# Kernel tuning notes

Measured on AMD Instinct MI355X. Metric: run time of the kernel, lower is better.

## Reference

```python
import jax, jax.numpy as jnp
import numpy as np

NEG_SLOPE = 0.2  # PyG GATConv default


def _gat_conv(x, src, dst, W, a_src, a_dst, bias, concat):
    # x: [N, F_in]; W: [H*C, F_in]; a_src/a_dst: [H, C]; src/dst: [E]
    n = x.shape[0]
    H, C = a_src.shape
    h = (x @ W.T).reshape(n, H, C)                       # [N, H, C]
    al_src = (h * a_src[None]).sum(-1)                   # [N, H]
    al_dst = (h * a_dst[None]).sum(-1)                   # [N, H]
    e = jax.nn.leaky_relu(al_src[src] + al_dst[dst], NEG_SLOPE)  # [E, H]
    # scatter-softmax over incoming edges of each dst node
    m = jax.ops.segment_max(e, dst, num_segments=n)      # [N, H]
    e = jnp.exp(e - m[dst])
    denom = jax.ops.segment_sum(e, dst, num_segments=n)  # [N, H]
    alpha = e / denom[dst]                               # [E, H]
    out = jax.ops.segment_sum(alpha[:, :, None] * h[src], dst, num_segments=n)  # [N, H, C]
    if concat:
        out = out.reshape(n, H * C)
    else:
        out = out.mean(axis=1)
    return out + bias


def setup_inputs() -> dict:
    key = jax.random.key(0)
    ks = jax.random.split(key, 16)
    N, E = 20000, 640000
    IN, HID, HEADS, OUT, HLSTM, NCLS = 256, 32, 4, 64, 32, 1
    s = 0.1
    return {
        "x": jax.random.normal(ks[0], (N, IN), jnp.float32),
        "conv1_w": jax.random.normal(ks[1], (HID * HEADS, IN), jnp.float32) * s,
        "conv1_att_src": jax.random.normal(ks[2], (HEADS, HID), jnp.float32) * s,
        "conv1_att_dst": jax.random.normal(ks[3], (HEADS, HID), jnp.float32) * s,
        "conv1_bias": jnp.zeros((HID * HEADS,), jnp.float32),
        "conv2_w": jax.random.normal(ks[4], (OUT, HID * HEADS), jnp.float32) * s,
        "conv2_att_src": jax.random.normal(ks[5], (1, OUT), jnp.float32) * s,
        "conv2_att_dst": jax.random.normal(ks[6], (1, OUT), jnp.float32) * s,
        "conv2_bias": jnp.zeros((OUT,), jnp.float32),
        "lstm_w_ih": jax.random.normal(ks[7], (4 * HLSTM, OUT), jnp.float32) * s,
        "lstm_w_hh": jax.random.normal(ks[8], (4 * HLSTM, HLSTM), jnp.float32) * s,
        "lstm_b_ih": jnp.zeros((4 * HLSTM,), jnp.float32),
        "lstm_b_hh": jnp.zeros((4 * HLSTM,), jnp.float32),
        "fc_w": jax.random.normal(ks[9], (NCLS, HLSTM), jnp.float32) * s,
        "fc_b": jnp.zeros((NCLS,), jnp.float32),
        "edge_index": jax.random.randint(ks[10], (2, E), 0, N, jnp.int64),
    }


def reference(x, conv1_w, conv1_att_src, conv1_att_dst, conv1_bias,
              conv2_w, conv2_att_src, conv2_att_dst, conv2_bias,
              lstm_w_ih, lstm_w_hh, lstm_b_ih, lstm_b_hh,
              fc_w, fc_b, edge_index):
    N = x.shape[0]
    loops = jnp.arange(N, dtype=edge_index.dtype)  # add_self_loops=True (PyG default)
    src = jnp.concatenate([edge_index[0], loops])
    dst = jnp.concatenate([edge_index[1], loops])

    h = _gat_conv(x, src, dst, conv1_w, conv1_att_src, conv1_att_dst, conv1_bias, concat=True)
    h = jax.nn.elu(h)
    h = _gat_conv(h, src, dst, conv2_w, conv2_att_src, conv2_att_dst, conv2_bias, concat=False)

    # LSTM over the node sequence, batch=1 (x.view(-1, N, out_dim))
    Hs = lstm_w_hh.shape[1]
    pre = h @ lstm_w_ih.T + (lstm_b_ih + lstm_b_hh)      # [N, 4H] input projections

    def step(carry, p):
        hp, cp = carry
        g = p + hp @ lstm_w_hh.T
        i, f, gg, o = jnp.split(g, 4)
        c = jax.nn.sigmoid(f) * cp + jax.nn.sigmoid(i) * jnp.tanh(gg)
        hn = jax.nn.sigmoid(o) * jnp.tanh(c)
        return (hn, c), hn

    init = (jnp.zeros((Hs,), x.dtype), jnp.zeros((Hs,), x.dtype))
    _, seq = jax.lax.scan(step, init, pre)               # [N, H]
    out = seq @ fc_w.T + fc_b                            # [N, num_classes]
    return out[None]                                     # [1, N, num_classes]
```

## Files before the change

kernel.cpp:

```cpp
#include <hip/hip_runtime.h>
#include <hip/hip_bf16.h>
#include <hip/hip_fp16.h>
#include <cstdint>
#include <cstddef>

#define LOG2E 1.44269504088896340736f
#define SLOTW 128
#define SCAP 32

typedef float v2f __attribute__((ext_vector_type(2)));
typedef _Float16 f16x8 __attribute__((ext_vector_type(8)));
typedef float f32x4 __attribute__((ext_vector_type(4)));

__global__ __launch_bounds__(256, 4)
void gemm1_mfma(const float* __restrict__ A, const float* __restrict__ B,
                const float* __restrict__ asrc, const float* __restrict__ adst,
                float* __restrict__ als, float* __restrict__ ald,
                __half* __restrict__ Ch, int N,
                const int* __restrict__ esrc, const int* __restrict__ edst,
                int* __restrict__ cnt, unsigned short* __restrict__ slots,
                int E, int gemmBlocks) {
  if ((int)blockIdx.x >= gemmBlocks) {
    const int part = (int)blockIdx.x & 7;
    const int PQ = (N + 7) >> 3;
    const int lo = part * PQ;
    const int hi = (lo + PQ < N) ? lo + PQ : N;
    const int sb = (int)blockIdx.x - gemmBlocks;
    const int chunk = sb >> 3;
    const int base = chunk * 1024 + (int)threadIdx.x * 4;
    if (base + 3 < E) {
      int4 ss = *(const int4*)(esrc + base);
      int4 dd = *(const int4*)(edst + base);
      if (dd.x >= lo && dd.x < hi) {
        int p = atomicAdd(&cnt[dd.x], 1);
        if (p < SCAP) slots[(size_t)dd.x * SLOTW + p] = (unsigned short)ss.x;
      }
      if (dd.y >= lo && dd.y < hi) {
        int p = atomicAdd(&cnt[N + dd.y], 1);
        if (p < SCAP) slots[(size_t)dd.y * SLOTW + 32 + p] = (unsigned short)ss.y;
      }
      if (dd.z >= lo && dd.z < hi) {
        int p = atomicAdd(&cnt[2 * N + dd.z], 1);
        if (p < SCAP) slots[(size_t)dd.z * SLOTW + 64 + p] = (unsigned short)ss.z;
      }
      if (dd.w >= lo && dd.w < hi) {
        int p = atomicAdd(&cnt[3 * N + dd.w], 1);
        if (p < SCAP) slots[(size_t)dd.w * SLOTW + 96 + p] = (unsigned short)ss.w;
      }
    } else if (base < E) {
      for (int t = base; t < E; ++t) {
        int s = esrc[t], d = edst[t];
        if (d < lo || d >= hi) continue;
        int j = t & 3;
        int pos = atomicAdd(&cnt[j * N + d], 1);
        if (pos < SCAP) slots[(size_t)d * SLOTW + j * 32 + pos] = (unsigned short)s;
      }
    }
    return;
  }
  constexpr int M = 128, K = 256, TN = 32, KB = 64;
  constexpr int LDH = 72;
  constexpr int RF = 2, CF = 2;
  constexpr int NS = K / KB;

  __shared__ __align__(16) _Float16 As[TN * LDH];
  __shared__ __align__(16) _Float16 Bs[M * LDH];

  const int tid = threadIdx.x;
  const int n0 = blockIdx.x * TN;
  const int w = tid >> 6, lane = tid & 63;
  const int lr = lane & 15, lg = lane >> 4;
  const int colbase = w * 32;

  const int ar = tid >> 3;
  const int ak = (tid & 7) * 8;
  const int gnA = n0 + ar;

  f32x4 acc[RF][CF];
#pragma unroll
  for (int rf = 0; rf < RF; ++rf)
#pragma unroll
    for (int cf = 0; cf < CF; ++cf) acc[rf][cf] = (f32x4){0.f, 0.f, 0.f, 0.f};

  float4 pa0, pa1;
  float4 pb[8];

  const float* aRow = A + (size_t)gnA * K + ak;

#define LOADG(k0)                                                              \
  do {                                                                         \
    if (gnA < N) { pa0 = *(const float4*)(aRow + (k0));                        \
                   pa1 = *(const float4*)(aRow + (k0) + 4); }                  \
    else { pa0 = make_float4(0.f,0.f,0.f,0.f); pa1 = pa0; }                    \
    _Pragma("unroll")                                                          \
    for (int c = 0; c < 4; ++c) {                                              \
      int cid = c * 256 + tid;                                                 \
      int brow = cid >> 3, bk = (cid & 7) * 8;                                 \
      const float* bp = B + (size_t)brow * K + (k0) + bk;                      \
      pb[2*c]   = *(const float4*)bp;                                          \
      pb[2*c+1] = *(const float4*)(bp + 4);                                    \
    }                                                                          \
  } while (0)

  LOADG(0);
  for (int s = 0; s < NS; ++s) {
    {
      f16x8 h;
      h[0]=(_Float16)pa0.x; h[1]=(_Float16)pa0.y; h[2]=(_Float16)pa0.z; h[3]=(_Float16)pa0.w;
      h[4]=(_Float16)pa1.x; h[5]=(_Float16)pa1.y; h[6]=(_Float16)pa1.z; h[7]=(_Float16)pa1.w;
      *(f16x8*)&As[ar * LDH + ak] = h;
#pragma unroll
      for (int c = 0; c < 4; ++c) {
        int cid = c * 256 + tid;
        int brow = cid >> 3, bk = (cid & 7) * 8;
        f16x8 hb;
        hb[0]=(_Float16)pb[2*c].x; hb[1]=(_Float16)pb[2*c].y;
        hb[2]=(_Float16)pb[2*c].z; hb[3]=(_Float16)pb[2*c].w;
        hb[4]=(_Float16)pb[2*c+1].x; hb[5]=(_Float16)pb[2*c+1].y;
        hb[6]=(_Float16)pb[2*c+1].z; hb[7]=(_Float16)pb[2*c+1].w;
        *(f16x8*)&Bs[brow * LDH + bk] = hb;
      }
    }
    __syncthreads();
    if (s + 1 < NS) LOADG((s + 1) * KB);
    {
      f16x8 af[2][RF], bf[2][CF];
#pragma unroll
      for (int ks = 0; ks < 2; ++ks) {
#pragma unroll
        for (int rf = 0; rf < RF; ++rf)
          af[ks][rf] = *(const f16x8*)&As[(rf * 16 + lr) * LDH + ks * 32 + 8 * lg];
#pragma unroll
        for (int cf = 0; cf < CF; ++cf)
          bf[ks][cf] = *(const f16x8*)&Bs[(colbase + cf * 16 + lr) * LDH + ks * 32 + 8 * lg];
      }
#pragma unroll
      for (int ks = 0; ks < 2; ++ks)
#pragma unroll
        for (int rf = 0; rf < RF; ++rf)
#pragma unroll
          for (int cf = 0; cf < CF; ++cf)
            acc[rf][cf] = __builtin_amdgcn_mfma_f32_16x16x32_f16(af[ks][rf], bf[ks][cf], acc[rf][cf], 0, 0, 0);
    }
    __syncthreads();
  }
#undef LOADG

#pragma unroll
  for (int rf = 0; rf < RF; ++rf) {
#pragma unroll
    for (int reg = 0; reg < 4; ++reg) {
      const int gr = n0 + rf * 16 + lg * 4 + reg;
      if (gr < N) {
#pragma unroll
        for (int cf = 0; cf < CF; ++cf)
          Ch[(size_t)gr * M + colbase + cf * 16 + lr] = __float2half(acc[rf][cf][reg]);
      }
    }
  }
  {
    float as_v[CF], ad_v[CF];
#pragma unroll
    for (int cf = 0; cf < CF; ++cf) {
      as_v[cf] = asrc[colbase + cf * 16 + lr];
      ad_v[cf] = adst[colbase + cf * 16 + lr];
    }
#pragma unroll
    for (int rf = 0; rf < RF; ++rf) {
#pragma unroll
      for (int reg = 0; reg < 4; ++reg) {
        const int gr = n0 + rf * 16 + lg * 4 + reg;
        float ps = acc[rf][0][reg] * as_v[0] + acc[rf][1][reg] * as_v[1];
        float pd = acc[rf][0][reg] * ad_v[0] + acc[rf][1][reg] * ad_v[1];
#pragma unroll
        for (int m = 1; m < 16; m <<= 1) { ps += __shfl_xor(ps, m); pd += __shfl_xor(pd, m); }
        if (lr == 0 && gr < N) {
          als[(size_t)gr * 4 + w] = ps;
          ald[(size_t)gr * 4 + w] = pd;
        }
      }
    }
  }
}

__global__ __launch_bounds__(256)
void gemm2_mfma(const float* __restrict__ A, const float* __restrict__ B,
                const float* __restrict__ asrc, const float* __restrict__ adst,
                float* __restrict__ als, float* __restrict__ ald,
                __half* __restrict__ Ch, int N) {
  constexpr int M = 64, K = 128, TN = 32, KB = 64;
  constexpr int LDH = 72;
  constexpr int RF = 2;
  constexpr int NS = K / KB;

  __shared__ __align__(16) _Float16 As[TN * LDH];
  __shared__ __align__(16) _Float16 Bs[M * LDH];
  __shared__ float alp_s[4][TN];
  __shared__ float alp_d[4][TN];

  const int tid = threadIdx.x;
  const int n0 = blockIdx.x * TN;
  const int w = tid >> 6, lane = tid & 63;
  const int lr = lane & 15, lg = lane >> 4;
  const int colbase = w * 16;

  const int ar = tid >> 3;
  const int ak = (tid & 7) * 8;
  const int gnA = n0 + ar;

  f32x4 acc[RF];
#pragma unroll
  for (int rf = 0; rf < RF; ++rf) acc[rf] = (f32x4){0.f, 0.f, 0.f, 0.f};

  float4 pa0, pa1;
  float4 pb[4];

  const float* aRow = A + (size_t)gnA * K + ak;

#define LOADG2(k0)                                                             \
  do {                                                                         \
    if (gnA < N) { pa0 = *(const float4*)(aRow + (k0));                        \
                   pa1 = *(const float4*)(aRow + (k0) + 4); }                  \
    else { pa0 = make_float4(0.f,0.f,0.f,0.f); pa1 = pa0; }                    \
    _Pragma("unroll")                                                          \
    for (int c = 0; c < 2; ++c) {                                              \
      int cid = c * 256 + tid;                                                 \
      int brow = cid >> 3, bk = (cid & 7) * 8;                                 \
      const float* bp = B + (size_t)brow * K + (k0) + bk;                      \
      pb[2*c]   = *(const float4*)bp;                                          \
      pb[2*c+1] = *(const float4*)(bp + 4);                                    \
    }                                                                          \
  } while (0)

  LOADG2(0);
  for (int s = 0; s < NS; ++s) {
    {
      f16x8 h;
      h[0]=(_Float16)pa0.x; h[1]=(_Float16)pa0.y; h[2]=(_Float16)pa0.z; h[3]=(_Float16)pa0.w;
      h[4]=(_Float16)pa1.x; h[5]=(_Float16)pa1.y; h[6]=(_Float16)pa1.z; h[7]=(_Float16)pa1.w;
      *(f16x8*)&As[ar * LDH + ak] = h;
#pragma unroll
      for (int c = 0; c < 2; ++c) {
        int cid = c * 256 + tid;
        int brow = cid >> 3, bk = (cid & 7) * 8;
        f16x8 hb;
        hb[0]=(_Float16)pb[2*c].x; hb[1]=(_Float16)pb[2*c].y;
        hb[2]=(_Float16)pb[2*c].z; hb[3]=(_Float16)pb[2*c].w;
        hb[4]=(_Float16)pb[2*c+1].x; hb[5]=(_Float16)pb[2*c+1].y;
        hb[6]=(_Float16)pb[2*c+1].z; hb[7]=(_Float16)pb[2*c+1].w;
        *(f16x8*)&Bs[brow * LDH + bk] = hb;
      }
    }
    __syncthreads();
    if (s + 1 < NS) LOADG2((s + 1) * KB);
    {
      f16x8 af[2][RF], bf[2];
#pragma unroll
      for (int ks = 0; ks < 2; ++ks) {
#pragma unroll
        for (int rf = 0; rf < RF; ++rf)
          af[ks][rf] = *(const f16x8*)&As[(rf * 16 + lr) * LDH + ks * 32 + 8 * lg];
        bf[ks] = *(const f16x8*)&Bs[(colbase + lr) * LDH + ks * 32 + 8 * lg];
      }
#pragma unroll
      for (int ks = 0; ks < 2; ++ks)
#pragma unroll
        for (int rf = 0; rf < RF; ++rf)
          acc[rf] = __builtin_amdgcn_mfma_f32_16x16x32_f16(af[ks][rf], bf[ks], acc[rf], 0, 0, 0);
    }
    __syncthreads();
  }
#undef LOADG2

  const float as_v = asrc[colbase + lr];
  const float ad_v = adst[colbase + lr];
#pragma unroll
  for (int rf = 0; rf < RF; ++rf) {
#pragma unroll
    for (int reg = 0; reg < 4; ++reg) {
      const int row = rf * 16 + lg * 4 + reg;
      const int gr = n0 + row;
      if (gr < N) Ch[(size_t)gr * M + colbase + lr] = __float2half(acc[rf][reg]);
      float ps = acc[rf][reg] * as_v;
      float pd = acc[rf][reg] * ad_v;
#pragma unroll
      for (int m = 1; m < 16; m <<= 1) { ps += __shfl_xor(ps, m); pd += __shfl_xor(pd, m); }
      if (lr == 0) { alp_s[w][row] = ps; alp_d[w][row] = pd; }
    }
  }
  __syncthreads();
  if (tid < TN) {
    const int gr = n0 + tid;
    if (gr < N) {
      als[gr] = alp_s[0][tid] + alp_s[1][tid] + alp_s[2][tid] + alp_s[3][tid];
      ald[gr] = alp_d[0][tid] + alp_d[1][tid] + alp_d[2][tid] + alp_d[3][tid];
    }
  }
}

__global__ __launch_bounds__(256)
void gemm3_mfma(const float* __restrict__ A, const float* __restrict__ B,
                const float* __restrict__ bias0, const float* __restrict__ bias1,
                float* __restrict__ C, int N) {
  constexpr int M = 128, K = 64, TN = 32;
  constexpr int LDH = 72;
  constexpr int RF = 2, CF = 2;

  __shared__ __align__(16) _Float16 Ahi[TN * LDH];
  __shared__ __align__(16) _Float16 Alo[TN * LDH];
  __shared__ __align__(16) _Float16 Bhi[M * LDH];
  __shared__ __align__(16) _Float16 Blo[M * LDH];

  const int tid = threadIdx.x;
  const int n0 = blockIdx.x * TN;
  const int w = tid >> 6, lane = tid & 63;
  const int lr = lane & 15, lg = lane >> 4;
  const int colbase = w * 32;

  {
    const int ar = tid >> 3, ak = (tid & 7) * 8;
    const int gn = n0 + ar;
    float v[8];
    if (gn < N) {
      float4 v0 = *(const float4*)(A + (size_t)gn * K + ak);
      float4 v1 = *(const float4*)(A + (size_t)gn * K + ak + 4);
      v[0]=v0.x; v[1]=v0.y; v[2]=v0.z; v[3]=v0.w; v[4]=v1.x; v[5]=v1.y; v[6]=v1.z; v[7]=v1.w;
    } else {
#pragma unroll
      for (int j = 0; j < 8; ++j) v[j] = 0.f;
    }
    f16x8 hh, hl;
#pragma unroll
    for (int j = 0; j < 8; ++j) {
      _Float16 h = (_Float16)v[j];
      hh[j] = h;
      hl[j] = (_Float16)(v[j] - (float)h);
    }
    *(f16x8*)&Ahi[ar * LDH + ak] = hh;
    *(f16x8*)&Alo[ar * LDH + ak] = hl;
  }
#pragma unroll
  for (int c = 0; c < 4; ++c) {
    const int cid = c * 256 + tid;
    const int brow = cid >> 3, bk = (cid & 7) * 8;
    float4 v0 = *(const float4*)(B + (size_t)brow * K + bk);
    float4 v1 = *(const float4*)(B + (size_t)brow * K + bk + 4);
    float v[8] = {v0.x, v0.y, v0.z, v0.w, v1.x, v1.y, v1.z, v1.w};
    f16x8 hh, hl;
#pragma unroll
    for (int j = 0; j < 8; ++j) {
      _Float16 h = (_Float16)v[j];
      hh[j] = h;
      hl[j] = (_Float16)(v[j] - (float)h);
    }
    *(f16x8*)&Bhi[brow * LDH + bk] = hh;
    *(f16x8*)&Blo[brow * LDH + bk] = hl;
  }
  __syncthreads();

  f32x4 acc[RF][CF];
#pragma unroll
  for (int rf = 0; rf < RF; ++rf)
#pragma unroll
    for (int cf = 0; cf < CF; ++cf) acc[rf][cf] = (f32x4){0.f, 0.f, 0.f, 0.f};

#pragma unroll
  for (int ks = 0; ks < 2; ++ks) {
    f16x8 ah[RF], al[RF], bh[CF], bl[CF];
#pragma unroll
    for (int rf = 0; rf < RF; ++rf) {
      ah[rf] = *(const f16x8*)&Ahi[(rf * 16 + lr) * LDH + ks * 32 + 8 * lg];
      al[rf] = *(const f16x8*)&Alo[(rf * 16 + lr) * LDH + ks * 32 + 8 * lg];
    }
#pragma unroll
    for (int cf = 0; cf < CF; ++cf) {
      bh[cf] = *(const f16x8*)&Bhi[(colbase + cf * 16 + lr) * LDH + ks * 32 + 8 * lg];
      bl[cf] = *(const f16x8*)&Blo[(colbase + cf * 16 + lr) * LDH + ks * 32 + 8 * lg];
    }
#pragma unroll
    for (int rf = 0; rf < RF; ++rf)
#pragma unroll
      for (int cf = 0; cf < CF; ++cf) {
        acc[rf][cf] = __builtin_amdgcn_mfma_f32_16x16x32_f16(ah[rf], bh[cf], acc[rf][cf], 0, 0, 0);
        acc[rf][cf] = __builtin_amdgcn_mfma_f32_16x16x32_f16(ah[rf], bl[cf], acc[rf][cf], 0, 0, 0);
        acc[rf][cf] = __builtin_amdgcn_mfma_f32_16x16x32_f16(al[rf], bh[cf], acc[rf][cf], 0, 0, 0);
      }
  }

  float bv[CF];
#pragma unroll
  for (int cf = 0; cf < CF; ++cf)
    bv[cf] = bias0[colbase + cf * 16 + lr] + bias1[colbase + cf * 16 + lr];
#pragma unroll
  for (int rf = 0; rf < RF; ++rf) {
#pragma unroll
    for (int reg = 0; reg < 4; ++reg) {
      const int gr = n0 + rf * 16 + lg * 4 + reg;
      if (gr < N) {
#pragma unroll
        for (int cf = 0; cf < CF; ++cf)
          C[(size_t)gr * M + colbase + cf * 16 + lr] = acc[rf][cf][reg] + bv[cf];
      }
    }
  }
}

template<int D, int H, bool ELU, int CAP>
__global__ __launch_bounds__(D)
void conv_edge(const __half* __restrict__ hsrc, const float* __restrict__ als,
               const float* __restrict__ ald, const float* __restrict__ bias,
               const int* __restrict__ cnt, const unsigned short* __restrict__ slots,
               const int* __restrict__ esrc, const int* __restrict__ edst, int E,
               float* __restrict__ out, int N) {
  constexpr int C = D / H;
  const int n = blockIdx.x;
  const int tid = threadIdx.x;
  const int myh = tid / C;
  const int c0 = cnt[n], c1 = cnt[N + n], c2 = cnt[2 * N + n], c3 = cnt[3 * N + n];
  const int deg_r = c0 + c1 + c2 + c3;
  const int deg = deg_r + 1;
  const bool ok = (c0 <= SCAP) && (c1 <= SCAP) && (c2 <= SCAP) && (c3 <= SCAP) && (deg <= CAP);

  __shared__ __align__(16) float lw[CAP][H];
  __shared__ int sidx[CAP];
  __shared__ float red[2][H];

  float ad[H];
#pragma unroll
  for (int hh = 0; hh < H; ++hh) ad[hh] = ald[(size_t)n * H + hh];

  float acc = 0.f;
  float myinv;
  if (ok) {
    const int b0 = c0, b1 = c0 + c1, b2 = b1 + c2;
    float sm[H];
#pragma unroll
    for (int hh = 0; hh < H; ++hh) sm[hh] = 0.f;
    const unsigned short* srow = slots + (size_t)n * SLOTW;
    for (int e = tid; e < deg; e += D) {
      int s;
      if (e == 0) s = n;
      else {
        int idx = e - 1, off;
        if (idx < b0)      off = idx;
        else if (idx < b1) off = 32 + (idx - b0);
        else if (idx < b2) off = 64 + (idx - b1);
        else               off = 96 + (idx - b2);
        s = (int)srow[off];
      }
      sidx[e] = s * (D * 2);
      if constexpr (H == 4) {
        float4 a4 = *(const float4*)(als + (size_t)s * 4);
        float l0 = a4.x + ad[0]; l0 = l0 > 0.f ? l0 : 0.2f * l0;
        float l1 = a4.y + ad[1]; l1 = l1 > 0.f ? l1 : 0.2f * l1;
        float l2 = a4.z + ad[2]; l2 = l2 > 0.f ? l2 : 0.2f * l2;
        float l3 = a4.w + ad[3]; l3 = l3 > 0.f ? l3 : 0.2f * l3;
        float w0 = __builtin_amdgcn_exp2f(LOG2E * l0);
        float w1 = __builtin_amdgcn_exp2f(LOG2E * l1);
        float w2 = __builtin_amdgcn_exp2f(LOG2E * l2);
        float w3 = __builtin_amdgcn_exp2f(LOG2E * l3);
        *(float4*)&lw[e][0] = make_float4(w0, w1, w2, w3);
        sm[0] += w0; sm[1] += w1; sm[2] += w2; sm[3] += w3;
      } else {
        float x = als[s] + ad[0];
        x = x > 0.f ? x : 0.2f * x;
        float w = __builtin_amdgcn_exp2f(LOG2E * x);
        lw[e][0] = w;
        sm[0] += w;
      }
    }
#pragma unroll
    for (int hh = 0; hh < H; ++hh) {
#pragma unroll
      for (int m = 32; m >= 1; m >>= 1) sm[hh] += __shfl_xor(sm[hh], m);
    }
    if constexpr (D > 64) {
      if ((tid & 63) == 0) {
#pragma unroll
        for (int hh = 0; hh < H; ++hh) red[tid >> 6][hh] = sm[hh];
      }
      __syncthreads();
#pragma unroll
      for (int hh = 0; hh < H; ++hh) sm[hh] = red[0][hh] + red[1][hh];
    }
    myinv = 1.0f / sm[myh];
    __syncthreads();
    const char* hb = (const char*)hsrc + (size_t)tid * 2;
#pragma unroll 8
    for (int e = 0; e < deg; ++e) {
      float w = lw[e][myh];
      int ofs = sidx[e];
      float hv = __half2float(*(const __half*)(hb + ofs));
      acc = fmaf(w, hv, acc);
    }
  } else {
    float mx[H];
#pragma unroll
    for (int hh = 0; hh < H; ++hh) {
      float xs_ = als[(size_t)n * H + hh] + ad[hh];
      xs_ = xs_ > 0.f ? xs_ : 0.2f * xs_;
      mx[hh] = xs_;
    }
    for (int e = tid; e < E; e += D) {
      if (edst[e] != n) continue;
      int s = esrc[e];
#pragma unroll
      for (int hh = 0; hh < H; ++hh) {
        float x = als[(size_t)s * H + hh] + ad[hh];
        x = x > 0.f ? x : 0.2f * x;
        mx[hh] = fmaxf(mx[hh], x);
      }
    }
#pragma unroll
    for (int hh = 0; hh < H; ++hh) {
#pragma unroll
      for (int m = 32; m >= 1; m >>= 1) mx[hh] = fmaxf(mx[hh], __shfl_xor(mx[hh], m));
    }
    if constexpr (D > 64) {
      if ((tid & 63) == 0) {
#pragma unroll
        for (int hh = 0; hh < H; ++hh) red[tid >> 6][hh] = mx[hh];
      }
      __syncthreads();
#pragma unroll
      for (int hh = 0; hh < H; ++hh) mx[hh] = fmaxf(red[0][hh], red[1][hh]);
      __syncthreads();
    }
    float sm[H];
#pragma unroll
    for (int hh = 0; hh < H; ++hh) sm[hh] = 0.f;
    if (tid == 0) {
#pragma unroll
      for (int hh = 0; hh < H; ++hh) {
        float x = als[(size_t)n * H + hh] + ad[hh];
        x = x > 0.f ? x : 0.2f * x;
        sm[hh] += __builtin_amdgcn_exp2f(LOG2E * (x - mx[hh]));
      }
    }
    for (int e = tid; e < E; e += D) {
      if (edst[e] != n) continue;
      int s = esrc[e];
#pragma unroll
      for (int hh = 0; hh < H; ++hh) {
        float x = als[(size_t)s * H + hh] + ad[hh];
        x = x > 0.f ? x : 0.2f * x;
        sm[hh] += __builtin_amdgcn_exp2f(LOG2E * (x - mx[hh]));
      }
    }
#pragma unroll
    for (int hh = 0; hh < H; ++hh) {
#pragma unroll
      for (int m = 32; m >= 1; m >>= 1) sm[hh] += __shfl_xor(sm[hh], m);
    }
    if constexpr (D > 64) {
      if ((tid & 63) == 0) {
#pragma unroll
        for (int hh = 0; hh < H; ++hh) red[tid >> 6][hh] = sm[hh];
      }
      __syncthreads();
#pragma unroll
      for (int hh = 0; hh < H; ++hh) sm[hh] = red[0][hh] + red[1][hh];
    }
    const float myad = ad[myh], mym = mx[myh];
    myinv = 1.0f / sm[myh];
    {
      float x = als[(size_t)n * H + myh] + myad;
      x = x > 0.f ? x : 0.2f * x;
      float w = __builtin_amdgcn_exp2f(LOG2E * (x - mym));
      acc = fmaf(w, __half2float(hsrc[(size_t)n * D + tid]), acc);
    }
    for (int e = 0; e < E; ++e) {
      if (edst[e] != n) continue;
      int s = esrc[e];
      float x = als[(size_t)s * H + myh] + myad;
      x = x > 0.f ? x : 0.2f * x;
      float w = __builtin_amdgcn_exp2f(LOG2E * (x - mym));
      acc = fmaf(w, __half2float(hsrc[(size_t)s * D + tid]), acc);
    }
  }
  float v = fmaf(acc, myinv, bias[tid]);
  if constexpr (ELU) v = v > 0.f ? v : (__builtin_amdgcn_exp2f(LOG2E * v) - 1.0f);
  out[(size_t)n * D + tid] = v;
}

#define LSTM_S 24
#define LSTM_W 64
__global__ __attribute__((amdgpu_waves_per_eu(1, 1))) __launch_bounds__(64)
void lstm_kernel(const float* __restrict__ pre, const float* __restrict__ whh,
                 const float* __restrict__ fcw, const float* __restrict__ fcb,
                 float* __restrict__ out, int N) {
  constexpr int U = 8;
  const int lane = threadIdx.x;
  const int k = lane & 31, half = lane >> 5;
  const int row0 = k + 32 * half;
  const int row1 = 64 + k + 32 * half;

  const int t0 = blockIdx.x * LSTM_S;
  const int tb = max(0, t0 - LSTM_W);
  const int te = min(t0 + LSTM_S, N);

  v2f wp[32];
#pragma unroll
  for (int j = 0; j < 32; ++j) {
    wp[j].x = whh[row0 * 32 + j];
    wp[j].y = whh[row1 * 32 + j];
  }
  const float mult_y = half ? -LOG2E : 2.0f * LOG2E;
  const float m1 = half ? 1.0f : -2.0f;
  const float a1c = half ? 0.0f : 1.0f;
  const float myfw = fcw[k];
  const float fcb0 = fcb[0];

  float hn = 0.f, cp = 0.f;
  float c0[U], c1[U], n0[U], n1[U];
  const float* pb = pre + (size_t)tb * 128;
#pragma unroll
  for (int u = 0; u < U; ++u) {
    c0[u] = pb[(size_t)u * 128 + row0];
    c1[u] = pb[(size_t)u * 128 + row1];
  }
#pragma unroll
  for (int u = 0; u < U; ++u) {
    n0[u] = pb[(size_t)(U + u) * 128 + row0];
    n1[u] = pb[(size_t)(U + u) * 128 + row1];
  }

#pragma unroll 1
  for (int t = tb; t < te; t += U) {
#pragma unroll
    for (int u = 0; u < U; ++u) {
      v2f acc0 = {c0[u], c1[u]};
      v2f acc1 = {0.f, 0.f}, acc2 = {0.f, 0.f}, acc3 = {0.f, 0.f};
      const int hni = __float_as_int(hn);
#pragma unroll
      for (int j = 0; j < 8; ++j) {
        float s = __int_as_float(__builtin_amdgcn_readlane(hni, 32 + j));
        v2f ss = {s, s};
        acc0 = __builtin_elementwise_fma(ss, wp[j], acc0);
      }
#pragma unroll
      for (int j = 8; j < 16; ++j) {
        float s = __int_as_float(__builtin_amdgcn_readlane(hni, 32 + j));
        v2f ss = {s, s};
        acc1 = __builtin_elementwise_fma(ss, wp[j], acc1);
      }
#pragma unroll
      for (int j = 16; j < 24; ++j) {
        float s = __int_as_float(__builtin_amdgcn_readlane(hni, 32 + j));
        v2f ss = {s, s};
        acc2 = __builtin_elementwise_fma(ss, wp[j], acc2);
      }
#pragma unroll
      for (int j = 24; j < 32; ++j) {
        float s = __int_as_float(__builtin_amdgcn_readlane(hni, 32 + j));
        v2f ss = {s, s};
        acc3 = __builtin_elementwise_fma(ss, wp[j], acc3);
      }
      v2f a01 = (acc0 + acc1) + (acc2 + acc3);
      float ax = a01.x;
      float ay = a01.y;
      float e0 = __builtin_amdgcn_exp2f(-LOG2E * ax);
      float sa = __builtin_amdgcn_rcpf(1.0f + e0);
      float e1 = __builtin_amdgcn_exp2f(mult_y * ay);
      float r1 = __builtin_amdgcn_rcpf(1.0f + e1);
      float v1 = fmaf(r1, m1, a1c);
      float op2 = half ? cp : v1;
      float q = sa * op2;
      float xu = __shfl_xor(q, 32, 64);
      float c = q + xu;
      cp = c;
      float e2 = __builtin_amdgcn_exp2f(2.0f * LOG2E * c);
      float r2 = __builtin_amdgcn_rcpf(1.0f + e2);
      float tc = fmaf(r2, -2.0f, 1.0f);
      hn = v1 * tc;
      const int tt = t + u;
      if (tt >= t0) {
        float p = hn * myfw;
        p += __shfl_xor(p, 16); p += __shfl_xor(p, 8); p += __shfl_xor(p, 4);
        p += __shfl_xor(p, 2);  p += __shfl_xor(p, 1);
        if (lane == 32) out[tt] = p + fcb0;
      }
    }
#pragma unroll
    for (int u = 0; u < U; ++u) { c0[u] = n0[u]; c1[u] = n1[u]; }
    const float* nx = pre + (size_t)(t + 2 * U) * 128;
#pragma unroll
    for (int u = 0; u < U; ++u) {
      n0[u] = nx[(size_t)u * 128 + row0];
      n1[u] = nx[(size_t)u * 128 + row1];
    }
  }
}

extern "C" void kernel_launch(void* const* d_in, const int* in_sizes, int n_in,
                              void* d_out, int out_size, void* d_ws, size_t ws_size,
                              hipStream_t stream) {
  const float* x   = (const float*)d_in[0];
  const float* w1  = (const float*)d_in[1];
  const float* a1s = (const float*)d_in[2];
  const float* a1d = (const float*)d_in[3];
  const float* b1  = (const float*)d_in[4];
  const float* w2  = (const float*)d_in[5];
  const float* a2s = (const float*)d_in[6];
  const float* a2d = (const float*)d_in[7];
  const float* b2  = (const float*)d_in[8];
  const float* wih = (const float*)d_in[9];
  const float* whh = (const float*)d_in[10];
  const float* bih = (const float*)d_in[11];
  const float* bhh = (const float*)d_in[12];
  const float* fcw = (const float*)d_in[13];
  const float* fcb = (const float*)d_in[14];
  const int*   ei  = (const int*)d_in[15];
  const int N = in_sizes[0] / 256;
  const int E = in_sizes[15] / 2;
  const int* esrc = ei;
  const int* edst = ei + E;

  float* fw = (float*)d_ws;
  size_t o = 0;
  __half* h1h = (__half*)(fw + o); o += (size_t)N * 64;
  __half* h2h = (__half*)(fw + o); o += (size_t)N * 32;
  float* x2   = fw + o; o += (size_t)N * 128;
  float* h3   = fw + o; o += (size_t)N * 64;
  float* pre  = fw + o; o += (size_t)(N + 16) * 128;
  float* al1s = fw + o; o += (size_t)N * 4;
  float* al1d = fw + o; o += (size_t)N * 4;
  float* al2s = fw + o; o += (size_t)N;
  float* al2d = fw + o; o += (size_t)N;
  int* cnt = (int*)(fw + o); o += (size_t)4 * N;
  unsigned short* slots = (unsigned short*)(fw + o);

  const int eb = (E + 1023) / 1024;
  const int gb1 = (N + 31) / 32;
  const int lstm_blocks = (N + LSTM_S - 1) / LSTM_S;

  hipMemsetAsync(cnt, 0, (size_t)4 * N * sizeof(int), stream);

  hipLaunchKernelGGL(gemm1_mfma, dim3(gb1 + 8 * eb), dim3(256), 0, stream,
                     x, w1, a1s, a1d, al1s, al1d, h1h, N,
                     esrc, edst, cnt, slots, E, gb1);

  hipLaunchKernelGGL((conv_edge<128, 4, true, 160>), dim3(N), dim3(128), 0, stream,
                     h1h, al1s, al1d, b1, cnt, slots, esrc, edst, E, x2, N);

  hipLaunchKernelGGL(gemm2_mfma, dim3(gb1), dim3(256), 0, stream,
                     x2, w2, a2s, a2d, al2s, al2d, h2h, N);

  hipLaunchKernelGGL((conv_edge<64, 1, false, 160>), dim3(N), dim3(64), 0, stream,
                     h2h, al2s, al2d, b2, cnt, slots, esrc, edst, E, h3, N);

  hipLaunchKernelGGL(gemm3_mfma, dim3(gb1), dim3(256), 0, stream,
                     h3, wih, bih, bhh, pre, N);

  hipLaunchKernelGGL(lstm_kernel, dim3(lstm_blocks), dim3(64), 0, stream,
                     pre, whh, fcw, fcb, (float*)d_out, N);
}
```

Measured before the change: 215.5 us.

## Replace global per-node atomic slotting with two-pass shared-memory bucket binning

Edge-to-slot construction moves from global per-node atomics, where each edge was processed by 8 partitioned blocks, to a block-local histogram over 64-node buckets. Each block reserves a range per bucket with one global atomic, then writes packed (local dst, src) words. A new csr_kernel then scatters each bucket into per-node slot rows using shared-memory counters. This removes most global atomic contention and the 4-way split counts, and simplifies index lookup in conv_edge. The cost is an extra kernel launch, an intermediate binned buffer, and a fixed bucket capacity that could overflow on skewed graphs.

```diff
diff --git a/kernel.cpp b/kernel.cpp
--- a/kernel.cpp
+++ b/kernel.cpp
@@ -6,7 +6,8 @@
 
 #define LOG2E 1.44269504088896340736f
 #define SLOTW 128
-#define SCAP 32
+#define BCAP  2816
+#define NBMAX 320
 
 typedef float v2f __attribute__((ext_vector_type(2)));
 typedef _Float16 f16x8 __attribute__((ext_vector_type(8)));
@@ -18,42 +19,57 @@
                 float* __restrict__ als, float* __restrict__ ald,
                 __half* __restrict__ Ch, int N,
                 const int* __restrict__ esrc, const int* __restrict__ edst,
-                int* __restrict__ cnt, unsigned short* __restrict__ slots,
+                int* __restrict__ bucket_cnt, unsigned int* __restrict__ binned,
                 int E, int gemmBlocks) {
   if ((int)blockIdx.x >= gemmBlocks) {
-    const int part = (int)blockIdx.x & 7;
-    const int PQ = (N + 7) >> 3;
-    const int lo = part * PQ;
-    const int hi = (lo + PQ < N) ? lo + PQ : N;
+    __shared__ int h_l[NBMAX], base_l[NBMAX], loc_l[NBMAX];
+    const int NB = (N + 63) >> 6;
     const int sb = (int)blockIdx.x - gemmBlocks;
-    const int chunk = sb >> 3;
-    const int base = chunk * 1024 + (int)threadIdx.x * 4;
-    if (base + 3 < E) {
-      int4 ss = *(const int4*)(esrc + base);
-      int4 dd = *(const int4*)(edst + base);
-      if (dd.x >= lo && dd.x < hi) {
-        int p = atomicAdd(&cnt[dd.x], 1);
-        if (p < SCAP) slots[(size_t)dd.x * SLOTW + p] = (unsigned short)ss.x;
-      }
-      if (dd.y >= lo && dd.y < hi) {
-        int p = atomicAdd(&cnt[N + dd.y], 1);
-        if (p < SCAP) slots[(size_t)dd.y * SLOTW + 32 + p] = (unsigned short)ss.y;
-      }
-      if (dd.z >= lo && dd.z < hi) {
-        int p = atomicAdd(&cnt[2 * N + dd.z], 1);
-        if (p < SCAP) slots[(size_t)dd.z * SLOTW + 64 + p] = (unsigned short)ss.z;
-      }
-      if (dd.w >= lo && dd.w < hi) {
-        int p = atomicAdd(&cnt[3 * N + dd.w], 1);
-        if (p < SCAP) slots[(size_t)dd.w * SLOTW + 96 + p] = (unsigned short)ss.w;
-      }
-    } else if (base < E) {
-      for (int t = base; t < E; ++t) {
-        int s = esrc[t], d = edst[t];
-        if (d < lo || d >= hi) continue;
-        int j = t & 3;
-        int pos = atomicAdd(&cnt[j * N + d], 1);
-        if (pos < SCAP) slots[(size_t)d * SLOTW + j * 32 + pos] = (unsigned short)s;
+    const int e0 = sb * 8192;
+    const int tid = threadIdx.x;
+    for (int i = tid; i < NB; i += 256) { h_l[i] = 0; loc_l[i] = 0; }
+    __syncthreads();
+#pragma unroll
+    for (int i = 0; i < 8; ++i) {
+      int e = e0 + i * 1024 + tid * 4;
+      if (e + 3 < E) {
+        int4 dd = *(const int4*)(edst + e);
+        atomicAdd(&h_l[dd.x >> 6], 1);
+        atomicAdd(&h_l[dd.y >> 6], 1);
+        atomicAdd(&h_l[dd.z >> 6], 1);
+        atomicAdd(&h_l[dd.w >> 6], 1);
+      } else {
+        for (int t = e; t < E && t < e + 4; ++t) atomicAdd(&h_l[edst[t] >> 6], 1);
+      }
+    }
+    __syncthreads();
+    for (int b = tid; b < NB; b += 256) {
+      int hv = h_l[b];
+      base_l[b] = hv ? atomicAdd(&bucket_cnt[b], hv) : 0;
+    }
+    __syncthreads();
+#pragma unroll
+    for (int i = 0; i < 8; ++i) {
+      int e = e0 + i * 1024 + tid * 4;
+      if (e + 3 < E) {
+        int4 ss = *(const int4*)(esrc + e);
+        int4 dd = *(const int4*)(edst + e);
+        int b0 = dd.x >> 6, b1 = dd.y >> 6, b2 = dd.z >> 6, b3 = dd.w >> 6;
+        int o0 = atomicAdd(&loc_l[b0], 1) + base_l[b0];
+        int o1 = atomicAdd(&loc_l[b1], 1) + base_l[b1];
+        int o2 = atomicAdd(&loc_l[b2], 1) + base_l[b2];
+        int o3 = atomicAdd(&loc_l[b3], 1) + base_l[b3];
+        if (o0 < BCAP) binned[(size_t)b0 * BCAP + o0] = ((unsigned)(dd.x & 63) << 16) | (unsigned)ss.x;
+        if (o1 < BCAP) binned[(size_t)b1 * BCAP + o1] = ((unsigned)(dd.y & 63) << 16) | (unsigned)ss.y;
+        if (o2 < BCAP) binned[(size_t)b2 * BCAP + o2] = ((unsigned)(dd.z & 63) << 16) | (unsigned)ss.z;
+        if (o3 < BCAP) binned[(size_t)b3 * BCAP + o3] = ((unsigned)(dd.w & 63) << 16) | (unsigned)ss.w;
+      } else {
+        for (int t = e; t < E && t < e + 4; ++t) {
+          int s = esrc[t], d = edst[t];
+          int b = d >> 6;
+          int o = atomicAdd(&loc_l[b], 1) + base_l[b];
+          if (o < BCAP) binned[(size_t)b * BCAP + o] = ((unsigned)(d & 63) << 16) | (unsigned)s;
+        }
       }
     }
     return;
@@ -184,6 +200,31 @@
 }
 
 __global__ __launch_bounds__(256)
+void csr_kernel(const unsigned int* __restrict__ binned, const int* __restrict__ bucket_cnt,
+                int* __restrict__ cnt, unsigned short* __restrict__ slots, int N) {
+  __shared__ int lcnt[64];
+  const int b = blockIdx.x;
+  const int tid = threadIdx.x;
+  if (tid < 64) lcnt[tid] = 0;
+  __syncthreads();
+  int m = bucket_cnt[b];
+  if (m > BCAP) m = BCAP;
+  const unsigned int* bp = binned + (size_t)b * BCAP;
+  for (int i = tid; i < m; i += 256) {
+    unsigned int v = bp[i];
+    int dl = (int)(v >> 16);
+    int s  = (int)(v & 0xFFFFu);
+    int pos = atomicAdd(&lcnt[dl], 1);
+    if (pos < SLOTW) slots[(size_t)(b * 64 + dl) * SLOTW + pos] = (unsigned short)s;
+  }
+  __syncthreads();
+  if (tid < 64) {
+    int n = b * 64 + tid;
+    if (n < N) cnt[n] = lcnt[tid];
+  }
+}
+
+__global__ __launch_bounds__(256)
 void gemm2_mfma(const float* __restrict__ A, const float* __restrict__ B,
                 const float* __restrict__ asrc, const float* __restrict__ adst,
                 float* __restrict__ als, float* __restrict__ ald,
@@ -416,10 +457,9 @@
   const int n = blockIdx.x;
   const int tid = threadIdx.x;
   const int myh = tid / C;
-  const int c0 = cnt[n], c1 = cnt[N + n], c2 = cnt[2 * N + n], c3 = cnt[3 * N + n];
-  const int deg_r = c0 + c1 + c2 + c3;
+  const int deg_r = cnt[n];
   const int deg = deg_r + 1;
-  const bool ok = (c0 <= SCAP) && (c1 <= SCAP) && (c2 <= SCAP) && (c3 <= SCAP) && (deg <= CAP);
+  const bool ok = (deg_r <= SLOTW) && (deg <= CAP);
 
   __shared__ __align__(16) float lw[CAP][H];
   __shared__ int sidx[CAP];
@@ -432,22 +472,12 @@
   float acc = 0.f;
   float myinv;
   if (ok) {
-    const int b0 = c0, b1 = c0 + c1, b2 = b1 + c2;
     float sm[H];
 #pragma unroll
     for (int hh = 0; hh < H; ++hh) sm[hh] = 0.f;
     const unsigned short* srow = slots + (size_t)n * SLOTW;
     for (int e = tid; e < deg; e += D) {
-      int s;
-      if (e == 0) s = n;
-      else {
-        int idx = e - 1, off;
-        if (idx < b0)      off = idx;
-        else if (idx < b1) off = 32 + (idx - b0);
-        else if (idx < b2) off = 64 + (idx - b1);
-        else               off = 96 + (idx - b2);
-        s = (int)srow[off];
-      }
+      int s = (e == 0) ? n : (int)srow[e - 1];
       sidx[e] = s * (D * 2);
       if constexpr (H == 4) {
         float4 a4 = *(const float4*)(als + (size_t)s * 4);
@@ -727,18 +757,24 @@
   float* al1d = fw + o; o += (size_t)N * 4;
   float* al2s = fw + o; o += (size_t)N;
   float* al2d = fw + o; o += (size_t)N;
-  int* cnt = (int*)(fw + o); o += (size_t)4 * N;
+  int* cnt = (int*)(fw + o); o += (size_t)N;
+  int* bucket_cnt = (int*)(fw + o); o += NBMAX;
+  unsigned int* binned = (unsigned int*)(fw + o); o += (size_t)NBMAX * BCAP;
   unsigned short* slots = (unsigned short*)(fw + o);
 
-  const int eb = (E + 1023) / 1024;
+  const int NB = (N + 63) >> 6;
+  const int binBlocks = (E + 8191) / 8192;
   const int gb1 = (N + 31) / 32;
   const int lstm_blocks = (N + LSTM_S - 1) / LSTM_S;
 
-  hipMemsetAsync(cnt, 0, (size_t)4 * N * sizeof(int), stream);
-
-  hipLaunchKernelGGL(gemm1_mfma, dim3(gb1 + 8 * eb), dim3(256), 0, stream,
+  hipMemsetAsync(bucket_cnt, 0, (size_t)NB * sizeof(int), stream);
+
+  hipLaunchKernelGGL(gemm1_mfma, dim3(gb1 + binBlocks), dim3(256), 0, stream,
                      x, w1, a1s, a1d, al1s, al1d, h1h, N,
-                     esrc, edst, cnt, slots, E, gb1);
+                     esrc, edst, bucket_cnt, binned, E, gb1);
+
+  hipLaunchKernelGGL(csr_kernel, dim3(NB), dim3(256), 0, stream,
+                     binned, bucket_cnt, cnt, slots, N);
 
   hipLaunchKernelGGL((conv_edge<128, 4, true, 160>), dim3(N), dim3(128), 0, stream,
                      h1h, al1s, al1d, b1, cnt, slots, esrc, edst, E, x2, N);
```

Result: faster. 205.2 us, median of 3 (-4.8%).
